# Optimization experiments

Hardware: AMD Instinct MI355X
Metric: run time of the kernel (lower is better)

Reference implementation:

```python
import jax, jax.numpy as jnp
import numpy as np

EPS = 1e-6

def setup_inputs() -> dict:
    key = jax.random.key(0)
    ks = jax.random.split(key, 6)
    N, E, Din, H, D = 50000, 800000, 256, 4, 32
    x = jax.random.normal(ks[0], (N, Din), dtype=jnp.float32)
    adj_indices = jax.random.randint(ks[1], (E, 2), 0, N, dtype=jnp.int32)
    adj_weights = jax.random.uniform(ks[2], (E,), dtype=jnp.float32)
    W = jax.random.normal(ks[3], (Din, H * D), dtype=jnp.float32) * (1.0 / np.sqrt(Din))
    a_src = jax.random.normal(ks[4], (H, D), dtype=jnp.float32)
    a_dst = jax.random.normal(ks[5], (H, D), dtype=jnp.float32)
    return {"x": x, "adj_indices": adj_indices, "adj_weights": adj_weights,
            "W": W, "a_src": a_src, "a_dst": a_dst}

def reference(x, adj_indices, adj_weights, W, a_src, a_dst):
    N = x.shape[0]
    H, D = a_src.shape
    h = (x @ W).reshape(N, H, D)                       # [N,H,D]
    src = adj_indices[:, 0]
    dst = adj_indices[:, 1]
    hs = h[src]                                        # [E,H,D]
    hd = h[dst]                                        # [E,H,D]
    raw = jnp.einsum('ehd,hd->eh', hs, a_src) + jnp.einsum('ehd,hd->eh', hd, a_dst)
    gate = jnp.clip(adj_weights, EPS, None)[:, None]   # [E,1]
    scores = jnp.tanh(raw) + jnp.log(gate)             # [E,H]
    # per-destination segment softmax (numerically stable)
    seg_max = jax.ops.segment_max(scores, dst, num_segments=N)   # [N,H]
    ex = jnp.exp(scores - seg_max[dst])
    denom = jax.ops.segment_sum(ex, dst, num_segments=N)         # [N,H]
    alpha = ex / denom[dst]                            # softmax over edges per dst
    alpha = alpha * gate
    messages = alpha[:, :, None] * hs                  # [E,H,D]
    out = jax.ops.segment_sum(messages, dst, num_segments=N)     # [N,H,D]
    out = out.reshape(N, H * D)
    return jax.nn.gelu(out, approximate=False)
```

## Files before the change

kernel.cpp:

```cpp
#include <hip/hip_runtime.h>
#include <hip/hip_bf16.h>

#define N_NODES 50000
#define N_EDGES 800000
#define DIN 256
#define HD 128
#define NH 4
#define CAP 64
#define CSTR 16

#define GROWS 64
#define LDKH 136

#define GEMM_BLOCKS ((N_NODES + GROWS - 1) / GROWS)
#define SCAT_BLOCKS ((N_EDGES + 255) / 256)

typedef __bf16 bf16x8 __attribute__((ext_vector_type(8)));
typedef float  f32x4  __attribute__((ext_vector_type(4)));

static __device__ __forceinline__ unsigned short f2bu(float v) {
  union { __hip_bfloat16 b; unsigned short u; } c;
  c.b = __float2bfloat16(v);
  return c.u;
}

static __device__ __forceinline__ unsigned short f2hu(float v) {
  union { _Float16 h; unsigned short u; } c;
  c.h = (_Float16)v;
  return c.u;
}

static __device__ __forceinline__ float hu2f(unsigned short u) {
  union { _Float16 h; unsigned short u; } c;
  c.u = u;
  return (float)c.h;
}

__global__ void init_kernel(const float* __restrict__ W,
                            unsigned short* __restrict__ Wt,
                            int* __restrict__ cursor) {
  int i = blockIdx.x * 256 + threadIdx.x;
  if (i < HD * DIN) {
    int c = i >> 8, k = i & 255;
    Wt[c * 256 + k] = f2bu(W[k * HD + c]);
  }
  if (i < N_NODES * CSTR) cursor[i] = 0;
}

__global__ __launch_bounds__(256, 4) void fused_gemm_scatter(
    const float* __restrict__ x,
    const unsigned short* __restrict__ Wt,
    const float* __restrict__ a_src,
    const float* __restrict__ a_dst,
    unsigned short* __restrict__ hbf,
    float* __restrict__ ssrc,
    float* __restrict__ sdst,
    const int2* __restrict__ adj,
    const float* __restrict__ wts,
    int* __restrict__ cursor,
    unsigned int* __restrict__ slots) {
  __shared__ unsigned short xs[GROWS * LDKH];
  const int tid = threadIdx.x;

  if (blockIdx.x >= GEMM_BLOCKS) {
    int e = (blockIdx.x - GEMM_BLOCKS) * 256 + tid;
    if (e >= N_EDGES) return;
    int2 sd = adj[e];
    if ((unsigned)sd.x >= (unsigned)N_NODES || (unsigned)sd.y >= (unsigned)N_NODES) return;
    float g = fmaxf(wts[e], 1e-6f);
    int pos = atomicAdd(&cursor[sd.y * CSTR], 1);
    if (pos >= CAP) pos = CAP - 1;
    unsigned packed = ((unsigned)f2hu(g) << 16) | (unsigned)sd.x;
    __builtin_nontemporal_store(packed, &slots[((size_t)sd.y << 6) + pos]);
    return;
  }

  const int row0 = blockIdx.x * GROWS;
  const int wid  = tid >> 6;
  const int lane = tid & 63;
  const int m    = lane & 15;
  const int q    = lane >> 4;

  f32x4 acc[8];
#pragma unroll
  for (int t = 0; t < 8; t++) acc[t] = (f32x4){0.f, 0.f, 0.f, 0.f};

#pragma unroll
  for (int ks = 0; ks < 2; ks++) {
#pragma unroll
    for (int it = 0; it < 8; it++) {
      int i  = it * 256 + tid;
      int r  = i >> 5;
      int kq = i & 31;
      int row = row0 + r;
      float4 v = make_float4(0.f, 0.f, 0.f, 0.f);
      if (row < N_NODES) v = *(const float4*)(x + (size_t)row * DIN + ks * 128 + 4 * kq);
      ushort4 b;
      b.x = f2bu(v.x); b.y = f2bu(v.y); b.z = f2bu(v.z); b.w = f2bu(v.w);
      *(ushort4*)&xs[r * LDKH + 4 * kq] = b;
    }
    __syncthreads();

    const unsigned short* xbase = &xs[(wid * 16 + m) * LDKH];
#pragma unroll
    for (int s = 0; s < 4; s++) {
      bf16x8 afrag = *(const bf16x8*)(xbase + 32 * s + 8 * q);
#pragma unroll
      for (int t = 0; t < 8; t++) {
        bf16x8 bfrag = *(const bf16x8*)(Wt + (size_t)(16 * t + m) * 256 + ks * 128 + 32 * s + 8 * q);
        acc[t] = __builtin_amdgcn_mfma_f32_16x16x32_bf16(afrag, bfrag, acc[t], 0, 0, 0);
      }
    }
    __syncthreads();
  }

#pragma unroll
  for (int t = 0; t < 8; t++) {
#pragma unroll
    for (int r = 0; r < 4; r++) {
      int row = row0 + wid * 16 + q * 4 + r;
      if (row < N_NODES) hbf[(size_t)row * HD + 16 * t + m] = f2bu(acc[t][r]);
    }
  }

  float as[8], ad[8];
#pragma unroll
  for (int t = 0; t < 8; t++) {
    as[t] = a_src[16 * t + m];
    ad[t] = a_dst[16 * t + m];
  }
#pragma unroll
  for (int r = 0; r < 4; r++) {
    float ps[NH] = {0.f, 0.f, 0.f, 0.f};
    float pd[NH] = {0.f, 0.f, 0.f, 0.f};
#pragma unroll
    for (int t = 0; t < 8; t++) {
      ps[t >> 1] = fmaf(acc[t][r], as[t], ps[t >> 1]);
      pd[t >> 1] = fmaf(acc[t][r], ad[t], pd[t >> 1]);
    }
#pragma unroll
    for (int mm = 8; mm >= 1; mm >>= 1) {
#pragma unroll
      for (int hh = 0; hh < NH; hh++) {
        ps[hh] += __shfl_xor(ps[hh], mm, 64);
        pd[hh] += __shfl_xor(pd[hh], mm, 64);
      }
    }
    int row = row0 + wid * 16 + q * 4 + r;
    if (m == 0 && row < N_NODES) {
#pragma unroll
      for (int hh = 0; hh < NH; hh++) {
        ssrc[row * NH + hh] = ps[hh];
        sdst[row * NH + hh] = pd[hh];
      }
    }
  }
}

__global__ __launch_bounds__(128, 8) void node_kernel(
    const int* __restrict__ cursor,
    const unsigned int* __restrict__ slots,
    const float4* __restrict__ ssrc4,
    const float4* __restrict__ sdst4,
    const unsigned int* __restrict__ hbf32,
    float* __restrict__ out) {
  const int tid  = threadIdx.x;
  const int wid  = tid >> 6;
  const int lane = tid & 63;
  const int n    = blockIdx.x * 2 + wid;
  const int hh   = lane >> 4;

  int deg = cursor[n * CSTR];
  if (deg > CAP) deg = CAP;

  __shared__ int    sidx[2][CAP];
  __shared__ float4 swv[2][CAP];

  float4 ex = make_float4(0.f, 0.f, 0.f, 0.f);
  if (lane < deg) {
    unsigned sl = slots[((size_t)n << 6) + lane];
    int s = (int)(sl & 0xffffu);
    float g = hu2f((unsigned short)(sl >> 16));
    float4 ss = ssrc4[s];
    float4 sd = sdst4[n];
    ex.x = g * expf(tanhf(ss.x + sd.x));
    ex.y = g * expf(tanhf(ss.y + sd.y));
    ex.z = g * expf(tanhf(ss.z + sd.z));
    ex.w = g * expf(tanhf(ss.w + sd.w));
    sidx[wid][lane] = s;
    swv[wid][lane] = make_float4(ex.x * g, ex.y * g, ex.z * g, ex.w * g);
  }

  float4 tot = ex;
#pragma unroll
  for (int mm = 32; mm >= 1; mm >>= 1) {
    tot.x += __shfl_xor(tot.x, mm, 64);
    tot.y += __shfl_xor(tot.y, mm, 64);
    tot.z += __shfl_xor(tot.z, mm, 64);
    tot.w += __shfl_xor(tot.w, mm, 64);
  }
  float dn  = (hh == 0) ? tot.x : (hh == 1) ? tot.y : (hh == 2) ? tot.z : tot.w;
  float inv = (dn > 0.f) ? 1.f / dn : 0.f;
  __syncthreads();

  float acc0 = 0.f, acc1 = 0.f;
  int j = 0;
  for (; j + 4 <= deg; j += 4) {
    int s0 = sidx[wid][j + 0], s1 = sidx[wid][j + 1];
    int s2 = sidx[wid][j + 2], s3 = sidx[wid][j + 3];
    unsigned u0 = hbf32[(size_t)s0 * (HD / 2) + lane];
    unsigned u1 = hbf32[(size_t)s1 * (HD / 2) + lane];
    unsigned u2 = hbf32[(size_t)s2 * (HD / 2) + lane];
    unsigned u3 = hbf32[(size_t)s3 * (HD / 2) + lane];
    float w0 = ((const float*)&swv[wid][j + 0])[hh];
    float w1 = ((const float*)&swv[wid][j + 1])[hh];
    float w2 = ((const float*)&swv[wid][j + 2])[hh];
    float w3 = ((const float*)&swv[wid][j + 3])[hh];
    acc0 = fmaf(w0, __uint_as_float(u0 << 16), acc0);
    acc1 = fmaf(w0, __uint_as_float(u0 & 0xffff0000u), acc1);
    acc0 = fmaf(w1, __uint_as_float(u1 << 16), acc0);
    acc1 = fmaf(w1, __uint_as_float(u1 & 0xffff0000u), acc1);
    acc0 = fmaf(w2, __uint_as_float(u2 << 16), acc0);
    acc1 = fmaf(w2, __uint_as_float(u2 & 0xffff0000u), acc1);
    acc0 = fmaf(w3, __uint_as_float(u3 << 16), acc0);
    acc1 = fmaf(w3, __uint_as_float(u3 & 0xffff0000u), acc1);
  }
  for (; j < deg; j++) {
    int s0 = sidx[wid][j];
    unsigned u0 = hbf32[(size_t)s0 * (HD / 2) + lane];
    float w0 = ((const float*)&swv[wid][j])[hh];
    acc0 = fmaf(w0, __uint_as_float(u0 << 16), acc0);
    acc1 = fmaf(w0, __uint_as_float(u0 & 0xffff0000u), acc1);
  }
  acc0 *= inv;
  acc1 *= inv;

  float2 gl;
  gl.x = 0.5f * acc0 * (1.f + erff(acc0 * 0.70710678118654752f));
  gl.y = 0.5f * acc1 * (1.f + erff(acc1 * 0.70710678118654752f));
  *(float2*)&out[(size_t)n * HD + 2 * lane] = gl;
}

extern "C" void kernel_launch(void* const* d_in, const int* in_sizes, int n_in,
                              void* d_out, int out_size, void* d_ws, size_t ws_size,
                              hipStream_t stream) {
  const float* x     = (const float*)d_in[0];
  const int2*  adj   = (const int2*)d_in[1];
  const float* wts   = (const float*)d_in[2];
  const float* W     = (const float*)d_in[3];
  const float* a_src = (const float*)d_in[4];
  const float* a_dst = (const float*)d_in[5];
  float* out = (float*)d_out;

  char* p = (char*)d_ws;
  auto carve = [&](size_t bytes) {
    char* q = p;
    p += (bytes + 255) & ~(size_t)255;
    return (void*)q;
  };
  unsigned short* hbf = (unsigned short*)carve((size_t)N_NODES * HD * sizeof(unsigned short));
  unsigned short* Wt  = (unsigned short*)carve((size_t)HD * DIN * sizeof(unsigned short));
  float* ssrc   = (float*)carve((size_t)N_NODES * NH * sizeof(float));
  float* sdst   = (float*)carve((size_t)N_NODES * NH * sizeof(float));
  unsigned int* slots = (unsigned int*)carve((size_t)N_NODES * CAP * sizeof(unsigned int));
  int*   cursor = (int*)carve((size_t)N_NODES * CSTR * sizeof(int));

  init_kernel<<<(N_NODES * CSTR + 255) / 256, 256, 0, stream>>>(W, Wt, cursor);
  fused_gemm_scatter<<<GEMM_BLOCKS + SCAT_BLOCKS, 256, 0, stream>>>(
      x, Wt, a_src, a_dst, hbf, ssrc, sdst, adj, wts, cursor, slots);
  node_kernel<<<N_NODES / 2, 128, 0, stream>>>(cursor, slots, (const float4*)ssrc,
                                               (const float4*)sdst,
                                               (const unsigned int*)hbf, out);
}
```

Measured before the change: 192.6 us.

## Replace global-atomic CSR slotting with two-pass shared-memory bucket sort by destination

Edge scatter no longer does one global atomic per edge into fixed 64-slot padded buckets. Each partition block bins 8192 edges by dst>>8 using shared-memory atomics. A new sort kernel then gathers each range, counting-sorts it by low byte and writes a compact CSR with offsets and degrees. The aim is to remove global atomic contention and the strided padded slot writes. The cost is an extra kernel launch, fixed cell capacities that can drop edges when a bin overflows, and a sort phase that runs only 196 blocks.

```diff
diff --git a/kernel.cpp b/kernel.cpp
--- a/kernel.cpp
+++ b/kernel.cpp
@@ -6,14 +6,17 @@
 #define DIN 256
 #define HD 128
 #define NH 4
-#define CAP 64
-#define CSTR 16
 
 #define GROWS 64
 #define LDKH 136
 
 #define GEMM_BLOCKS ((N_NODES + GROWS - 1) / GROWS)
-#define SCAT_BLOCKS ((N_EDGES + 255) / 256)
+
+#define EPB   8192
+#define PBLKS ((N_EDGES + EPB - 1) / EPB)
+#define RNG   196
+#define CELLC 112
+#define MAXT  6144
 
 typedef __bf16 bf16x8 __attribute__((ext_vector_type(8)));
 typedef float  f32x4  __attribute__((ext_vector_type(4)));
@@ -38,13 +41,15 @@
 
 __global__ void init_kernel(const float* __restrict__ W,
                             unsigned short* __restrict__ Wt,
-                            int* __restrict__ cursor) {
+                            unsigned int* __restrict__ counts,
+                            unsigned int* __restrict__ gctr) {
   int i = blockIdx.x * 256 + threadIdx.x;
   if (i < HD * DIN) {
     int c = i >> 8, k = i & 255;
     Wt[c * 256 + k] = f2bu(W[k * HD + c]);
   }
-  if (i < N_NODES * CSTR) cursor[i] = 0;
+  if (i < PBLKS * RNG) counts[i] = 0;
+  if (i == 0) *gctr = 0;
 }
 
 __global__ __launch_bounds__(256, 4) void fused_gemm_scatter(
@@ -57,21 +62,37 @@
     float* __restrict__ sdst,
     const int2* __restrict__ adj,
     const float* __restrict__ wts,
-    int* __restrict__ cursor,
-    unsigned int* __restrict__ slots) {
+    unsigned int* __restrict__ bins_sg,
+    unsigned char* __restrict__ bins_fd,
+    unsigned int* __restrict__ counts) {
   __shared__ unsigned short xs[GROWS * LDKH];
+  __shared__ unsigned int offs[RNG];
   const int tid = threadIdx.x;
 
   if (blockIdx.x >= GEMM_BLOCKS) {
-    int e = (blockIdx.x - GEMM_BLOCKS) * 256 + tid;
-    if (e >= N_EDGES) return;
-    int2 sd = adj[e];
-    if ((unsigned)sd.x >= (unsigned)N_NODES || (unsigned)sd.y >= (unsigned)N_NODES) return;
-    float g = fmaxf(wts[e], 1e-6f);
-    int pos = atomicAdd(&cursor[sd.y * CSTR], 1);
-    if (pos >= CAP) pos = CAP - 1;
-    unsigned packed = ((unsigned)f2hu(g) << 16) | (unsigned)sd.x;
-    __builtin_nontemporal_store(packed, &slots[((size_t)sd.y << 6) + pos]);
+    const int pid = blockIdx.x - GEMM_BLOCKS;
+    for (int i = tid; i < RNG; i += 256) offs[i] = 0;
+    __syncthreads();
+    const int e0 = pid * EPB;
+    for (int i = 0; i < EPB / 256; i++) {
+      int e = e0 + i * 256 + tid;
+      if (e < N_EDGES) {
+        int2 sd = adj[e];
+        if ((unsigned)sd.x < (unsigned)N_NODES && (unsigned)sd.y < (unsigned)N_NODES) {
+          float g = fmaxf(wts[e], 1e-6f);
+          int r = sd.y >> 8;
+          unsigned pos = atomicAdd(&offs[r], 1u);
+          if (pos < CELLC) {
+            size_t cell = ((size_t)pid * RNG + r) * CELLC + pos;
+            bins_sg[cell] = ((unsigned)f2hu(g) << 16) | (unsigned)(sd.x & 0xffff);
+            bins_fd[cell] = (unsigned char)(sd.y & 255);
+          }
+        }
+      }
+    }
+    __syncthreads();
+    for (int r = tid; r < RNG; r += 256)
+      counts[pid * RNG + r] = (offs[r] < CELLC) ? offs[r] : CELLC;
     return;
   }
 
@@ -157,8 +178,74 @@
   }
 }
 
+__global__ __launch_bounds__(256, 2) void sort_kernel(
+    const unsigned int* __restrict__ counts,
+    const unsigned int* __restrict__ bins_sg,
+    const unsigned char* __restrict__ bins_fd,
+    unsigned int* __restrict__ slots,
+    unsigned int* __restrict__ off_out,
+    int* __restrict__ deg_out,
+    unsigned int* __restrict__ gctr) {
+  const int b   = blockIdx.x;
+  const int tid = threadIdx.x;
+
+  __shared__ unsigned int  cnt[PBLKS];
+  __shared__ unsigned int  pfxp[PBLKS + 1];
+  __shared__ unsigned int  sg[MAXT];
+  __shared__ unsigned char fdv[MAXT];
+  __shared__ unsigned int  h2[256], pfx2[256], c2[256];
+  __shared__ unsigned int  baseS, totalS;
+
+  if (tid < PBLKS) cnt[tid] = counts[(size_t)tid * RNG + b];
+  if (tid < 256) { h2[tid] = 0; c2[tid] = 0; }
+  __syncthreads();
+  if (tid == 0) {
+    unsigned s = 0;
+    for (int p = 0; p < PBLKS; p++) { pfxp[p] = s; s += cnt[p]; }
+    pfxp[PBLKS] = s;
+    totalS = (s < MAXT) ? s : MAXT;
+  }
+  __syncthreads();
+  const unsigned total = totalS;
+
+  for (unsigned k = tid; k < total; k += 256) {
+    int lo = 0, hi = PBLKS - 1;
+    while (lo < hi) { int mid = (lo + hi + 1) >> 1; if (pfxp[mid] <= k) lo = mid; else hi = mid - 1; }
+    unsigned j = k - pfxp[lo];
+    size_t cell = ((size_t)lo * RNG + b) * CELLC + j;
+    sg[k]  = bins_sg[cell];
+    fdv[k] = bins_fd[cell];
+  }
+  __syncthreads();
+
+  for (unsigned k = tid; k < total; k += 256) atomicAdd(&h2[fdv[k]], 1u);
+  __syncthreads();
+
+  if (tid == 0) {
+    unsigned s = 0;
+    for (int i = 0; i < 256; i++) { pfx2[i] = s; s += h2[i]; }
+    baseS = atomicAdd(gctr, s);
+  }
+  __syncthreads();
+  const unsigned base = baseS;
+
+  int nloc = N_NODES - b * 256;
+  if (nloc > 256) nloc = 256;
+  if (tid < nloc) {
+    off_out[b * 256 + tid] = base + pfx2[tid];
+    deg_out[b * 256 + tid] = (int)h2[tid];
+  }
+
+  for (unsigned k = tid; k < total; k += 256) {
+    unsigned f = fdv[k];
+    unsigned pos = atomicAdd(&c2[f], 1u);
+    slots[base + pfx2[f] + pos] = sg[k];
+  }
+}
+
 __global__ __launch_bounds__(128, 8) void node_kernel(
-    const int* __restrict__ cursor,
+    const unsigned int* __restrict__ off_in,
+    const int* __restrict__ deg_in,
     const unsigned int* __restrict__ slots,
     const float4* __restrict__ ssrc4,
     const float4* __restrict__ sdst4,
@@ -170,15 +257,16 @@
   const int n    = blockIdx.x * 2 + wid;
   const int hh   = lane >> 4;
 
-  int deg = cursor[n * CSTR];
-  if (deg > CAP) deg = CAP;
-
-  __shared__ int    sidx[2][CAP];
-  __shared__ float4 swv[2][CAP];
+  int deg = deg_in[n];
+  if (deg > 64) deg = 64;
+  unsigned off = off_in[n];
+
+  __shared__ int    sidx[2][64];
+  __shared__ float4 swv[2][64];
 
   float4 ex = make_float4(0.f, 0.f, 0.f, 0.f);
   if (lane < deg) {
-    unsigned sl = slots[((size_t)n << 6) + lane];
+    unsigned sl = slots[off + lane];
     int s = (int)(sl & 0xffffu);
     float g = hu2f((unsigned short)(sl >> 16));
     float4 ss = ssrc4[s];
@@ -262,13 +350,19 @@
   unsigned short* Wt  = (unsigned short*)carve((size_t)HD * DIN * sizeof(unsigned short));
   float* ssrc   = (float*)carve((size_t)N_NODES * NH * sizeof(float));
   float* sdst   = (float*)carve((size_t)N_NODES * NH * sizeof(float));
-  unsigned int* slots = (unsigned int*)carve((size_t)N_NODES * CAP * sizeof(unsigned int));
-  int*   cursor = (int*)carve((size_t)N_NODES * CSTR * sizeof(int));
-
-  init_kernel<<<(N_NODES * CSTR + 255) / 256, 256, 0, stream>>>(W, Wt, cursor);
-  fused_gemm_scatter<<<GEMM_BLOCKS + SCAT_BLOCKS, 256, 0, stream>>>(
-      x, Wt, a_src, a_dst, hbf, ssrc, sdst, adj, wts, cursor, slots);
-  node_kernel<<<N_NODES / 2, 128, 0, stream>>>(cursor, slots, (const float4*)ssrc,
+  unsigned int*  bins_sg = (unsigned int*)carve((size_t)PBLKS * RNG * CELLC * sizeof(unsigned int));
+  unsigned char* bins_fd = (unsigned char*)carve((size_t)PBLKS * RNG * CELLC);
+  unsigned int*  counts  = (unsigned int*)carve((size_t)PBLKS * RNG * sizeof(unsigned int));
+  unsigned int*  slots   = (unsigned int*)carve((size_t)N_EDGES * sizeof(unsigned int));
+  unsigned int*  off_arr = (unsigned int*)carve((size_t)N_NODES * sizeof(unsigned int));
+  int*           deg_arr = (int*)carve((size_t)N_NODES * sizeof(int));
+  unsigned int*  gctr    = (unsigned int*)carve(sizeof(unsigned int));
+
+  init_kernel<<<(HD * DIN + 255) / 256, 256, 0, stream>>>(W, Wt, counts, gctr);
+  fused_gemm_scatter<<<GEMM_BLOCKS + PBLKS, 256, 0, stream>>>(
+      x, Wt, a_src, a_dst, hbf, ssrc, sdst, adj, wts, bins_sg, bins_fd, counts);
+  sort_kernel<<<RNG, 256, 0, stream>>>(counts, bins_sg, bins_fd, slots, off_arr, deg_arr, gctr);
+  node_kernel<<<N_NODES / 2, 128, 0, stream>>>(off_arr, deg_arr, slots, (const float4*)ssrc,
                                                (const float4*)sdst,
                                                (const unsigned int*)hbf, out);
 }
```

After: 218.9 us. 13.6% more time.
